# Kernel tuning notes

Measured on AMD Instinct MI355X. Metric: run time of the kernel, lower is better.

Reference implementation:

```python
import jax, jax.numpy as jnp
import numpy as np

N = 100_000   # nodes
E = 1_600_000 # edges (avg degree 16)
D = 64        # embed/hidden dim
V = 50_000    # vocab
G = 128       # graphs in batch
C = 20        # classes


def setup_inputs() -> dict:
    key = jax.random.key(0)
    ks = jax.random.split(key, 11)
    tokens = jax.random.randint(ks[0], (N,), 0, V)
    edge_src = jax.random.randint(ks[1], (E,), 0, N)
    edge_dst = jax.random.randint(ks[2], (E,), 0, N)
    graph_ids = jnp.sort(jax.random.randint(ks[3], (N,), 0, G))
    s = 1.0 / np.sqrt(D)
    return {
        "tokens": tokens,
        "edge_src": edge_src,
        "edge_dst": edge_dst,
        "graph_ids": graph_ids,
        "emb_table": jax.random.normal(ks[4], (V, D), jnp.float32) * 0.02,
        "W1": jax.random.normal(ks[5], (D, D), jnp.float32) * s,
        "b1": jax.random.normal(ks[6], (D,), jnp.float32) * s,
        "W2": jax.random.normal(ks[7], (D, D), jnp.float32) * s,
        "b2": jax.random.normal(ks[8], (D,), jnp.float32) * s,
        "Wc": jax.random.normal(ks[9], (D, C), jnp.float32) * s,
        "bc": jax.random.normal(ks[10], (C,), jnp.float32) * s,
    }


def reference(tokens, edge_src, edge_dst, graph_ids, emb_table, W1, b1, W2, b2, Wc, bc):
    # Embedding lookup: [N, D]
    h = emb_table[tokens]
    # in-degree per dst node (zero-degree nodes get 0 features, like DGL mean)
    deg = jax.ops.segment_sum(jnp.ones((E,), h.dtype), edge_dst, num_segments=N)
    inv_deg = (1.0 / jnp.maximum(deg, 1.0))[:, None]  # [N,1]

    def gcn(h, W, b):
        # copy_src + mean: gather src feats, segment-sum into dst, divide by degree
        agg = jax.ops.segment_sum(h[edge_src], edge_dst, num_segments=N) * inv_deg
        return jax.nn.relu(agg @ W + b)

    h = gcn(h, W1, b1)
    h = gcn(h, W2, b2)

    # dgl.mean_nodes: per-graph mean pooling
    cnt = jax.ops.segment_sum(jnp.ones((N,), h.dtype), graph_ids, num_segments=G)
    hg = jax.ops.segment_sum(h, graph_ids, num_segments=G) / jnp.maximum(cnt, 1.0)[:, None]
    return hg @ Wc + bc  # [G, C] logits
```

## Files before the change

### kernel.cpp

```cpp
#include <hip/hip_runtime.h>

#define DIM 64
#define CLS 20
#define SCAN_T 256
#define SCAN_E 1024

__global__ void deg_count_kernel(const int* __restrict__ edst, int* __restrict__ deg, int E) {
    int e = blockIdx.x * blockDim.x + threadIdx.x;
    if (e < E) atomicAdd(&deg[edst[e]], 1);
}

__global__ void scan1_kernel(const int* __restrict__ deg, int* __restrict__ rp,
                             int* __restrict__ bsum, int N) {
    __shared__ int sh[SCAN_T];
    int base = blockIdx.x * SCAN_E + threadIdx.x * 4;
    int v0 = (base + 0 < N) ? deg[base + 0] : 0;
    int v1 = (base + 1 < N) ? deg[base + 1] : 0;
    int v2 = (base + 2 < N) ? deg[base + 2] : 0;
    int v3 = (base + 3 < N) ? deg[base + 3] : 0;
    sh[threadIdx.x] = v0 + v1 + v2 + v3;
    __syncthreads();
    for (int off = 1; off < SCAN_T; off <<= 1) {
        int t = (threadIdx.x >= off) ? sh[threadIdx.x - off] : 0;
        __syncthreads();
        sh[threadIdx.x] += t;
        __syncthreads();
    }
    int run = (threadIdx.x > 0) ? sh[threadIdx.x - 1] : 0;
    if (base + 0 < N) rp[base + 0] = run; run += v0;
    if (base + 1 < N) rp[base + 1] = run; run += v1;
    if (base + 2 < N) rp[base + 2] = run; run += v2;
    if (base + 3 < N) rp[base + 3] = run;
    if (threadIdx.x == SCAN_T - 1) bsum[blockIdx.x] = sh[SCAN_T - 1];
}

__global__ void scan2_kernel(int* __restrict__ bsum, int NB) {
    __shared__ int sh[128];
    int v = (threadIdx.x < NB) ? bsum[threadIdx.x] : 0;
    sh[threadIdx.x] = v;
    __syncthreads();
    for (int off = 1; off < 128; off <<= 1) {
        int t = (threadIdx.x >= off) ? sh[threadIdx.x - off] : 0;
        __syncthreads();
        sh[threadIdx.x] += t;
        __syncthreads();
    }
    if (threadIdx.x < NB) bsum[threadIdx.x] = sh[threadIdx.x] - v;
}

__global__ void scan3_kernel(int* __restrict__ rp, const int* __restrict__ bsum, int N) {
    int i = blockIdx.x * blockDim.x + threadIdx.x;
    if (i < N) rp[i] += bsum[i >> 10];
}

__global__ void scatter_kernel(const int* __restrict__ esrc, const int* __restrict__ edst,
                               int* __restrict__ cursor, int* __restrict__ csr_src, int E) {
    int e = blockIdx.x * blockDim.x + threadIdx.x;
    if (e < E) {
        int pos = atomicAdd(&cursor[edst[e]], 1);
        csr_src[pos] = esrc[e];
    }
}

__global__ void embed_kernel(const int* __restrict__ tokens, const float* __restrict__ emb,
                             float* __restrict__ h, int N) {
    int t = blockIdx.x * blockDim.x + threadIdx.x;
    int n = t >> 4, c = t & 15;
    if (n < N) {
        int tok = tokens[n];
        ((float4*)h)[(size_t)n * 16 + c] = ((const float4*)emb)[(size_t)tok * 16 + c];
    }
}

__global__ void agg_csr_kernel(const int* __restrict__ rp, const int* __restrict__ deg,
                               const int* __restrict__ csr_src, const float* __restrict__ h,
                               float* __restrict__ agg, int N) {
    int t = blockIdx.x * blockDim.x + threadIdx.x;
    int n = t >> 4, c = t & 15;
    if (n >= N) return;
    int beg = rp[n], end = beg + deg[n];
    float ax = 0.f, ay = 0.f, az = 0.f, aw = 0.f;
    for (int e = beg; e < end; ++e) {
        int s = csr_src[e];
        float4 v = ((const float4*)h)[(size_t)s * 16 + c];
        ax += v.x; ay += v.y; az += v.z; aw += v.w;
    }
    float4 o = {ax, ay, az, aw};
    ((float4*)agg)[(size_t)n * 16 + c] = o;
}

__global__ void gemm_relu_kernel(const float* __restrict__ agg, const int* __restrict__ deg,
                                 const float* __restrict__ W, const float* __restrict__ b,
                                 float* __restrict__ out, int N) {
    __shared__ float4 Ws[64 * 16];
    __shared__ float4 bs[16];
    for (int i = threadIdx.x; i < 64 * 16; i += blockDim.x) Ws[i] = ((const float4*)W)[i];
    if (threadIdx.x < 16) bs[threadIdx.x] = ((const float4*)b)[threadIdx.x];
    __syncthreads();
    int n = blockIdx.x * blockDim.x + threadIdx.x;
    if (n >= N) return;
    float inv = 1.0f / fmaxf((float)deg[n], 1.0f);
    float4 hv[16];
    #pragma unroll
    for (int j = 0; j < 16; ++j) hv[j] = ((const float4*)agg)[(size_t)n * 16 + j];
    float4 acc[16];
    #pragma unroll
    for (int j = 0; j < 16; ++j) { acc[j].x = 0.f; acc[j].y = 0.f; acc[j].z = 0.f; acc[j].w = 0.f; }
    #pragma unroll
    for (int k4 = 0; k4 < 16; ++k4) {
        float4 hq = hv[k4];
        #pragma unroll
        for (int kk = 0; kk < 4; ++kk) {
            float hk = (kk == 0) ? hq.x : (kk == 1) ? hq.y : (kk == 2) ? hq.z : hq.w;
            int k = k4 * 4 + kk;
            #pragma unroll
            for (int j = 0; j < 16; ++j) {
                float4 w = Ws[k * 16 + j];
                acc[j].x = fmaf(hk, w.x, acc[j].x);
                acc[j].y = fmaf(hk, w.y, acc[j].y);
                acc[j].z = fmaf(hk, w.z, acc[j].z);
                acc[j].w = fmaf(hk, w.w, acc[j].w);
            }
        }
    }
    #pragma unroll
    for (int j = 0; j < 16; ++j) {
        float4 bb = bs[j];
        float4 o;
        o.x = fmaxf(fmaf(inv, acc[j].x, bb.x), 0.f);
        o.y = fmaxf(fmaf(inv, acc[j].y, bb.y), 0.f);
        o.z = fmaxf(fmaf(inv, acc[j].z, bb.z), 0.f);
        o.w = fmaxf(fmaf(inv, acc[j].w, bb.w), 0.f);
        ((float4*)out)[(size_t)n * 16 + j] = o;
    }
}

__device__ __forceinline__ int lower_bound_i(const int* a, int n, int key) {
    int lo = 0, hi = n;
    while (lo < hi) {
        int mid = (lo + hi) >> 1;
        if (a[mid] < key) lo = mid + 1; else hi = mid;
    }
    return lo;
}

__global__ void pool_head_kernel(const float* __restrict__ h, const int* __restrict__ gids,
                                 const float* __restrict__ Wc, const float* __restrict__ bc,
                                 float* __restrict__ out, int N) {
    __shared__ float4 red[256];
    __shared__ float hg[64];
    int g = blockIdx.x;
    int lo = lower_bound_i(gids, N, g);
    int hi = lower_bound_i(gids, N, g + 1);
    int r = threadIdx.x >> 4, c = threadIdx.x & 15;
    float ax = 0.f, ay = 0.f, az = 0.f, aw = 0.f;
    for (int n = lo + r; n < hi; n += 16) {
        float4 v = ((const float4*)h)[(size_t)n * 16 + c];
        ax += v.x; ay += v.y; az += v.z; aw += v.w;
    }
    float4 a = {ax, ay, az, aw};
    red[threadIdx.x] = a;
    __syncthreads();
    for (int s = 8; s > 0; s >>= 1) {
        if (r < s) {
            float4 m = red[r * 16 + c];
            float4 o = red[(r + s) * 16 + c];
            m.x += o.x; m.y += o.y; m.z += o.z; m.w += o.w;
            red[r * 16 + c] = m;
        }
        __syncthreads();
    }
    if (r == 0) {
        float icnt = 1.0f / fmaxf((float)(hi - lo), 1.0f);
        float4 m = red[c];
        hg[c * 4 + 0] = m.x * icnt;
        hg[c * 4 + 1] = m.y * icnt;
        hg[c * 4 + 2] = m.z * icnt;
        hg[c * 4 + 3] = m.w * icnt;
    }
    __syncthreads();
    if (threadIdx.x < CLS) {
        float s = bc[threadIdx.x];
        #pragma unroll
        for (int k = 0; k < 64; ++k) s = fmaf(hg[k], Wc[k * CLS + threadIdx.x], s);
        out[(size_t)g * CLS + threadIdx.x] = s;
    }
}

extern "C" void kernel_launch(void* const* d_in, const int* in_sizes, int n_in,
                              void* d_out, int out_size, void* d_ws, size_t ws_size,
                              hipStream_t stream) {
    const int*   tokens = (const int*)d_in[0];
    const int*   esrc   = (const int*)d_in[1];
    const int*   edst   = (const int*)d_in[2];
    const int*   gids   = (const int*)d_in[3];
    const float* emb    = (const float*)d_in[4];
    const float* W1     = (const float*)d_in[5];
    const float* b1     = (const float*)d_in[6];
    const float* W2     = (const float*)d_in[7];
    const float* b2     = (const float*)d_in[8];
    const float* Wc     = (const float*)d_in[9];
    const float* bc     = (const float*)d_in[10];
    int N = in_sizes[0];
    int E = in_sizes[1];
    float* out = (float*)d_out;

    float* h      = (float*)d_ws;
    float* agg    = h + (size_t)N * 64;
    int*   deg    = (int*)(agg + (size_t)N * 64);
    int*   rp     = deg + N;
    int*   cursor = rp + N;
    int*   csr    = cursor + N;
    int*   bsum   = csr + E;

    int NB = (N + SCAN_E - 1) / SCAN_E;

    hipMemsetAsync(deg, 0, (size_t)N * sizeof(int), stream);

    deg_count_kernel<<<(E + 255) / 256, 256, 0, stream>>>(edst, deg, E);
    scan1_kernel<<<NB, SCAN_T, 0, stream>>>(deg, rp, bsum, N);
    scan2_kernel<<<1, 128, 0, stream>>>(bsum, NB);
    scan3_kernel<<<(N + 255) / 256, 256, 0, stream>>>(rp, bsum, N);
    hipMemcpyAsync(cursor, rp, (size_t)N * sizeof(int), hipMemcpyDeviceToDevice, stream);
    scatter_kernel<<<(E + 255) / 256, 256, 0, stream>>>(esrc, edst, cursor, csr, E);

    embed_kernel<<<(N * 16 + 255) / 256, 256, 0, stream>>>(tokens, emb, h, N);

    agg_csr_kernel<<<(N * 16 + 255) / 256, 256, 0, stream>>>(rp, deg, csr, h, agg, N);
    gemm_relu_kernel<<<(N + 255) / 256, 256, 0, stream>>>(agg, deg, W1, b1, h, N);

    agg_csr_kernel<<<(N * 16 + 255) / 256, 256, 0, stream>>>(rp, deg, csr, h, agg, N);
    gemm_relu_kernel<<<(N + 255) / 256, 256, 0, stream>>>(agg, deg, W2, b2, h, N);

    pool_head_kernel<<<128, 256, 0, stream>>>(h, gids, Wc, bc, out, N);
}
```

Baseline: 512.8 us.

## Partition degree count and CSR scatter atomics into destination bands

```diff
diff --git a/kernel.cpp b/kernel.cpp
--- a/kernel.cpp
+++ b/kernel.cpp
@@ -4,10 +4,46 @@
 #define CLS 20
 #define SCAN_T 256
 #define SCAN_E 1024
-
-__global__ void deg_count_kernel(const int* __restrict__ edst, int* __restrict__ deg, int E) {
-    int e = blockIdx.x * blockDim.x + threadIdx.x;
-    if (e < E) atomicAdd(&deg[edst[e]], 1);
+#define NBANDS 8
+#define BBLOCKS 1024
+
+__global__ void banded_count_kernel(const int* __restrict__ edst, int* __restrict__ deg,
+                                    int N, int E) {
+    int band   = blockIdx.x & (NBANDS - 1);
+    int chunk  = blockIdx.x >> 3;
+    int nchunk = gridDim.x >> 3;
+    int bandSize = (N + NBANDS - 1) / NBANDS;
+    int lo = band * bandSize;
+    int hi = min(lo + bandSize, N);
+    int per  = (E + nchunk - 1) / nchunk;
+    int ebeg = chunk * per;
+    int eend = min(ebeg + per, E);
+    for (int e = ebeg + threadIdx.x; e < eend; e += blockDim.x) {
+        int d = edst[e];
+        if (d >= lo && d < hi) atomicAdd(&deg[d], 1);
+    }
+}
+
+__global__ void banded_scatter_kernel(const int* __restrict__ esrc, const int* __restrict__ edst,
+                                      int* __restrict__ cursor, int* __restrict__ csr_src,
+                                      int N, int E) {
+    int band   = blockIdx.x & (NBANDS - 1);
+    int chunk  = blockIdx.x >> 3;
+    int nchunk = gridDim.x >> 3;
+    int bandSize = (N + NBANDS - 1) / NBANDS;
+    int lo = band * bandSize;
+    int hi = min(lo + bandSize, N);
+    int per  = (E + nchunk - 1) / nchunk;
+    int ebeg = chunk * per;
+    int eend = min(ebeg + per, E);
+    for (int e = ebeg + threadIdx.x; e < eend; e += blockDim.x) {
+        int d = edst[e];
+        int s = esrc[e];
+        if (d >= lo && d < hi) {
+            int pos = atomicAdd(&cursor[d], 1);
+            csr_src[pos] = s;
+        }
+    }
 }
 
 __global__ void scan1_kernel(const int* __restrict__ deg, int* __restrict__ rp,
@@ -48,17 +84,13 @@
     if (threadIdx.x < NB) bsum[threadIdx.x] = sh[threadIdx.x] - v;
 }
 
-__global__ void scan3_kernel(int* __restrict__ rp, const int* __restrict__ bsum, int N) {
+__global__ void scan3_kernel(int* __restrict__ rp, int* __restrict__ cursor,
+                             const int* __restrict__ bsum, int N) {
     int i = blockIdx.x * blockDim.x + threadIdx.x;
-    if (i < N) rp[i] += bsum[i >> 10];
-}
-
-__global__ void scatter_kernel(const int* __restrict__ esrc, const int* __restrict__ edst,
-                               int* __restrict__ cursor, int* __restrict__ csr_src, int E) {
-    int e = blockIdx.x * blockDim.x + threadIdx.x;
-    if (e < E) {
-        int pos = atomicAdd(&cursor[edst[e]], 1);
-        csr_src[pos] = esrc[e];
+    if (i < N) {
+        int v = rp[i] + bsum[i >> 10];
+        rp[i] = v;
+        cursor[i] = v;
     }
 }
 
@@ -217,12 +249,11 @@
 
     hipMemsetAsync(deg, 0, (size_t)N * sizeof(int), stream);
 
-    deg_count_kernel<<<(E + 255) / 256, 256, 0, stream>>>(edst, deg, E);
+    banded_count_kernel<<<BBLOCKS, 256, 0, stream>>>(edst, deg, N, E);
     scan1_kernel<<<NB, SCAN_T, 0, stream>>>(deg, rp, bsum, N);
     scan2_kernel<<<1, 128, 0, stream>>>(bsum, NB);
-    scan3_kernel<<<(N + 255) / 256, 256, 0, stream>>>(rp, bsum, N);
-    hipMemcpyAsync(cursor, rp, (size_t)N * sizeof(int), hipMemcpyDeviceToDevice, stream);
-    scatter_kernel<<<(E + 255) / 256, 256, 0, stream>>>(esrc, edst, cursor, csr, E);
+    scan3_kernel<<<(N + 255) / 256, 256, 0, stream>>>(rp, cursor, bsum, N);
+    banded_scatter_kernel<<<BBLOCKS, 256, 0, stream>>>(esrc, edst, cursor, csr, N, E);
 
     embed_kernel<<<(N * 16 + 255) / 256, 256, 0, stream>>>(tokens, emb, h, N);
 
```

Measured after the change: 459.8 us. -10.3%, faster.

## Replace CSR build with bucketed edge queues and fuse aggregation with GEMM

Applied to the files above, without the earlier changes.

```diff
diff --git a/kernel.cpp b/kernel.cpp
--- a/kernel.cpp
+++ b/kernel.cpp
@@ -2,63 +2,37 @@
 
 #define DIM 64
 #define CLS 20
-#define SCAN_T 256
-#define SCAN_E 1024
-
-__global__ void deg_count_kernel(const int* __restrict__ edst, int* __restrict__ deg, int E) {
-    int e = blockIdx.x * blockDim.x + threadIdx.x;
-    if (e < E) atomicAdd(&deg[edst[e]], 1);
-}
-
-__global__ void scan1_kernel(const int* __restrict__ deg, int* __restrict__ rp,
-                             int* __restrict__ bsum, int N) {
-    __shared__ int sh[SCAN_T];
-    int base = blockIdx.x * SCAN_E + threadIdx.x * 4;
-    int v0 = (base + 0 < N) ? deg[base + 0] : 0;
-    int v1 = (base + 1 < N) ? deg[base + 1] : 0;
-    int v2 = (base + 2 < N) ? deg[base + 2] : 0;
-    int v3 = (base + 3 < N) ? deg[base + 3] : 0;
-    sh[threadIdx.x] = v0 + v1 + v2 + v3;
-    __syncthreads();
-    for (int off = 1; off < SCAN_T; off <<= 1) {
-        int t = (threadIdx.x >= off) ? sh[threadIdx.x - off] : 0;
-        __syncthreads();
-        sh[threadIdx.x] += t;
-        __syncthreads();
-    }
-    int run = (threadIdx.x > 0) ? sh[threadIdx.x - 1] : 0;
-    if (base + 0 < N) rp[base + 0] = run; run += v0;
-    if (base + 1 < N) rp[base + 1] = run; run += v1;
-    if (base + 2 < N) rp[base + 2] = run; run += v2;
-    if (base + 3 < N) rp[base + 3] = run;
-    if (threadIdx.x == SCAN_T - 1) bsum[blockIdx.x] = sh[SCAN_T - 1];
-}
-
-__global__ void scan2_kernel(int* __restrict__ bsum, int NB) {
-    __shared__ int sh[128];
-    int v = (threadIdx.x < NB) ? bsum[threadIdx.x] : 0;
-    sh[threadIdx.x] = v;
-    __syncthreads();
-    for (int off = 1; off < 128; off <<= 1) {
-        int t = (threadIdx.x >= off) ? sh[threadIdx.x - off] : 0;
-        __syncthreads();
-        sh[threadIdx.x] += t;
-        __syncthreads();
-    }
-    if (threadIdx.x < NB) bsum[threadIdx.x] = sh[threadIdx.x] - v;
-}
-
-__global__ void scan3_kernel(int* __restrict__ rp, const int* __restrict__ bsum, int N) {
-    int i = blockIdx.x * blockDim.x + threadIdx.x;
-    if (i < N) rp[i] += bsum[i >> 10];
-}
-
-__global__ void scatter_kernel(const int* __restrict__ esrc, const int* __restrict__ edst,
-                               int* __restrict__ cursor, int* __restrict__ csr_src, int E) {
-    int e = blockIdx.x * blockDim.x + threadIdx.x;
-    if (e < E) {
-        int pos = atomicAdd(&cursor[edst[e]], 1);
-        csr_src[pos] = esrc[e];
+#define BSZ 160
+#define MAXBND 640
+#define QCAP 3072
+#define PCHUNK 4096
+#define ASTRIDE 68
+
+__global__ void init_qcur_kernel(int* __restrict__ qcur, int nbnd) {
+    int i = threadIdx.x;
+    if (i < nbnd) qcur[i] = i * QCAP;
+}
+
+__global__ __launch_bounds__(512) void partition_kernel(
+        const int* __restrict__ esrc, const int* __restrict__ edst,
+        int2* __restrict__ queue, int* __restrict__ qcur, int nbnd, int E) {
+    __shared__ int hist[MAXBND];
+    __shared__ int pc[MAXBND];
+    int cbeg = blockIdx.x * PCHUNK;
+    int cend = min(cbeg + PCHUNK, E);
+    for (int i = threadIdx.x; i < nbnd; i += blockDim.x) hist[i] = 0;
+    __syncthreads();
+    for (int e = cbeg + threadIdx.x; e < cend; e += blockDim.x)
+        atomicAdd(&hist[edst[e] / BSZ], 1);
+    __syncthreads();
+    for (int i = threadIdx.x; i < nbnd; i += blockDim.x)
+        pc[i] = hist[i] ? atomicAdd(&qcur[i], hist[i]) : 0;
+    __syncthreads();
+    for (int e = cbeg + threadIdx.x; e < cend; e += blockDim.x) {
+        int d = edst[e];
+        int s = esrc[e];
+        int pos = atomicAdd(&pc[d / BSZ], 1);
+        queue[pos] = make_int2(s, d);
     }
 }
 
@@ -72,66 +46,87 @@
     }
 }
 
-__global__ void agg_csr_kernel(const int* __restrict__ rp, const int* __restrict__ deg,
-                               const int* __restrict__ csr_src, const float* __restrict__ h,
-                               float* __restrict__ agg, int N) {
-    int t = blockIdx.x * blockDim.x + threadIdx.x;
-    int n = t >> 4, c = t & 15;
-    if (n >= N) return;
-    int beg = rp[n], end = beg + deg[n];
-    float ax = 0.f, ay = 0.f, az = 0.f, aw = 0.f;
-    for (int e = beg; e < end; ++e) {
-        int s = csr_src[e];
-        float4 v = ((const float4*)h)[(size_t)s * 16 + c];
-        ax += v.x; ay += v.y; az += v.z; aw += v.w;
-    }
-    float4 o = {ax, ay, az, aw};
-    ((float4*)agg)[(size_t)n * 16 + c] = o;
-}
-
-__global__ void gemm_relu_kernel(const float* __restrict__ agg, const int* __restrict__ deg,
-                                 const float* __restrict__ W, const float* __restrict__ b,
-                                 float* __restrict__ out, int N) {
+__global__ __launch_bounds__(512) void fused_layer_kernel(
+        const int2* __restrict__ queue, const int* __restrict__ qcur,
+        const float* __restrict__ hin, const float* __restrict__ W,
+        const float* __restrict__ bias, float* __restrict__ hout, int N) {
+    __shared__ float  acc[BSZ * ASTRIDE];
+    __shared__ int    ldeg[BSZ];
     __shared__ float4 Ws[64 * 16];
-    __shared__ float4 bs[16];
-    for (int i = threadIdx.x; i < 64 * 16; i += blockDim.x) Ws[i] = ((const float4*)W)[i];
-    if (threadIdx.x < 16) bs[threadIdx.x] = ((const float4*)b)[threadIdx.x];
-    __syncthreads();
-    int n = blockIdx.x * blockDim.x + threadIdx.x;
-    if (n >= N) return;
-    float inv = 1.0f / fmaxf((float)deg[n], 1.0f);
-    float4 hv[16];
-    #pragma unroll
-    for (int j = 0; j < 16; ++j) hv[j] = ((const float4*)agg)[(size_t)n * 16 + j];
-    float4 acc[16];
-    #pragma unroll
-    for (int j = 0; j < 16; ++j) { acc[j].x = 0.f; acc[j].y = 0.f; acc[j].z = 0.f; acc[j].w = 0.f; }
-    #pragma unroll
-    for (int k4 = 0; k4 < 16; ++k4) {
-        float4 hq = hv[k4];
-        #pragma unroll
-        for (int kk = 0; kk < 4; ++kk) {
-            float hk = (kk == 0) ? hq.x : (kk == 1) ? hq.y : (kk == 2) ? hq.z : hq.w;
-            int k = k4 * 4 + kk;
+    __shared__ float4 bs4[16];
+    int tid = threadIdx.x;
+
+    for (int i = tid; i < BSZ * (ASTRIDE / 4); i += blockDim.x) {
+        float4 z = {0.f, 0.f, 0.f, 0.f};
+        int r = i / (ASTRIDE / 4), q = i % (ASTRIDE / 4);
+        *(float4*)&acc[r * ASTRIDE + q * 4] = z;
+    }
+    for (int i = tid; i < BSZ; i += blockDim.x) ldeg[i] = 0;
+    for (int i = tid; i < 64 * 16; i += blockDim.x) Ws[i] = ((const float4*)W)[i];
+    if (tid < 16) bs4[tid] = ((const float4*)bias)[tid];
+    __syncthreads();
+
+    int b = blockIdx.x;
+    int nbase = b * BSZ;
+    int qbeg = b * QCAP;
+    int qend = qcur[b];
+    int slot = tid >> 4, c = tid & 15;
+
+    int e = qbeg + slot;
+    for (; e + 32 < qend; e += 64) {
+        int2 e0 = queue[e];
+        int2 e1 = queue[e + 32];
+        float4 v0 = ((const float4*)hin)[(size_t)e0.x * 16 + c];
+        float4 v1 = ((const float4*)hin)[(size_t)e1.x * 16 + c];
+        float* a0 = &acc[(e0.y - nbase) * ASTRIDE + c * 4];
+        atomicAdd(a0 + 0, v0.x); atomicAdd(a0 + 1, v0.y);
+        atomicAdd(a0 + 2, v0.z); atomicAdd(a0 + 3, v0.w);
+        if (c == 0) atomicAdd(&ldeg[e0.y - nbase], 1);
+        float* a1 = &acc[(e1.y - nbase) * ASTRIDE + c * 4];
+        atomicAdd(a1 + 0, v1.x); atomicAdd(a1 + 1, v1.y);
+        atomicAdd(a1 + 2, v1.z); atomicAdd(a1 + 3, v1.w);
+        if (c == 0) atomicAdd(&ldeg[e1.y - nbase], 1);
+    }
+    if (e < qend) {
+        int2 e0 = queue[e];
+        float4 v0 = ((const float4*)hin)[(size_t)e0.x * 16 + c];
+        float* a0 = &acc[(e0.y - nbase) * ASTRIDE + c * 4];
+        atomicAdd(a0 + 0, v0.x); atomicAdd(a0 + 1, v0.y);
+        atomicAdd(a0 + 2, v0.z); atomicAdd(a0 + 3, v0.w);
+        if (c == 0) atomicAdd(&ldeg[e0.y - nbase], 1);
+    }
+    __syncthreads();
+
+    for (int r0 = 0; r0 < BSZ; r0 += 32) {
+        int r = r0 + slot;
+        int n = nbase + r;
+        if (n < N) {
+            float inv = 1.0f / fmaxf((float)ldeg[r], 1.0f);
+            float sx = 0.f, sy = 0.f, sz = 0.f, sw = 0.f;
             #pragma unroll
-            for (int j = 0; j < 16; ++j) {
-                float4 w = Ws[k * 16 + j];
-                acc[j].x = fmaf(hk, w.x, acc[j].x);
-                acc[j].y = fmaf(hk, w.y, acc[j].y);
-                acc[j].z = fmaf(hk, w.z, acc[j].z);
-                acc[j].w = fmaf(hk, w.w, acc[j].w);
+            for (int k4 = 0; k4 < 16; ++k4) {
+                float4 aq = *(const float4*)&acc[r * ASTRIDE + k4 * 4];
+                float4 w0 = Ws[(k4 * 4 + 0) * 16 + c];
+                float4 w1 = Ws[(k4 * 4 + 1) * 16 + c];
+                float4 w2 = Ws[(k4 * 4 + 2) * 16 + c];
+                float4 w3 = Ws[(k4 * 4 + 3) * 16 + c];
+                sx = fmaf(aq.x, w0.x, sx); sy = fmaf(aq.x, w0.y, sy);
+                sz = fmaf(aq.x, w0.z, sz); sw = fmaf(aq.x, w0.w, sw);
+                sx = fmaf(aq.y, w1.x, sx); sy = fmaf(aq.y, w1.y, sy);
+                sz = fmaf(aq.y, w1.z, sz); sw = fmaf(aq.y, w1.w, sw);
+                sx = fmaf(aq.z, w2.x, sx); sy = fmaf(aq.z, w2.y, sy);
+                sz = fmaf(aq.z, w2.z, sz); sw = fmaf(aq.z, w2.w, sw);
+                sx = fmaf(aq.w, w3.x, sx); sy = fmaf(aq.w, w3.y, sy);
+                sz = fmaf(aq.w, w3.z, sz); sw = fmaf(aq.w, w3.w, sw);
             }
+            float4 bb = bs4[c];
+            float4 o;
+            o.x = fmaxf(fmaf(inv, sx, bb.x), 0.f);
+            o.y = fmaxf(fmaf(inv, sy, bb.y), 0.f);
+            o.z = fmaxf(fmaf(inv, sz, bb.z), 0.f);
+            o.w = fmaxf(fmaf(inv, sw, bb.w), 0.f);
+            ((float4*)hout)[(size_t)n * 16 + c] = o;
         }
-    }
-    #pragma unroll
-    for (int j = 0; j < 16; ++j) {
-        float4 bb = bs[j];
-        float4 o;
-        o.x = fmaxf(fmaf(inv, acc[j].x, bb.x), 0.f);
-        o.y = fmaxf(fmaf(inv, acc[j].y, bb.y), 0.f);
-        o.z = fmaxf(fmaf(inv, acc[j].z, bb.z), 0.f);
-        o.w = fmaxf(fmaf(inv, acc[j].w, bb.w), 0.f);
-        ((float4*)out)[(size_t)n * 16 + j] = o;
     }
 }
 
@@ -205,32 +200,17 @@
     int E = in_sizes[1];
     float* out = (float*)d_out;
 
-    float* h      = (float*)d_ws;
-    float* agg    = h + (size_t)N * 64;
-    int*   deg    = (int*)(agg + (size_t)N * 64);
-    int*   rp     = deg + N;
-    int*   cursor = rp + N;
-    int*   csr    = cursor + N;
-    int*   bsum   = csr + E;
-
-    int NB = (N + SCAN_E - 1) / SCAN_E;
-
-    hipMemsetAsync(deg, 0, (size_t)N * sizeof(int), stream);
-
-    deg_count_kernel<<<(E + 255) / 256, 256, 0, stream>>>(edst, deg, E);
-    scan1_kernel<<<NB, SCAN_T, 0, stream>>>(deg, rp, bsum, N);
-    scan2_kernel<<<1, 128, 0, stream>>>(bsum, NB);
-    scan3_kernel<<<(N + 255) / 256, 256, 0, stream>>>(rp, bsum, N);
-    hipMemcpyAsync(cursor, rp, (size_t)N * sizeof(int), hipMemcpyDeviceToDevice, stream);
-    scatter_kernel<<<(E + 255) / 256, 256, 0, stream>>>(esrc, edst, cursor, csr, E);
-
-    embed_kernel<<<(N * 16 + 255) / 256, 256, 0, stream>>>(tokens, emb, h, N);
-
-    agg_csr_kernel<<<(N * 16 + 255) / 256, 256, 0, stream>>>(rp, deg, csr, h, agg, N);
-    gemm_relu_kernel<<<(N + 255) / 256, 256, 0, stream>>>(agg, deg, W1, b1, h, N);
-
-    agg_csr_kernel<<<(N * 16 + 255) / 256, 256, 0, stream>>>(rp, deg, csr, h, agg, N);
-    gemm_relu_kernel<<<(N + 255) / 256, 256, 0, stream>>>(agg, deg, W2, b2, h, N);
-
-    pool_head_kernel<<<128, 256, 0, stream>>>(h, gids, Wc, bc, out, N);
-}
+    int nbnd = (N + BSZ - 1) / BSZ;
+
+    float* hA    = (float*)d_ws;
+    float* hB    = hA + (size_t)N * 64;
+    int2*  queue = (int2*)(hB + (size_t)N * 64);
+    int*   qcur  = (int*)(queue + (size_t)MAXBND * QCAP);
+
+    init_qcur_kernel<<<1, MAXBND, 0, stream>>>(qcur, nbnd);
+    partition_kernel<<<(E + PCHUNK - 1) / PCHUNK, 512, 0, stream>>>(esrc, edst, queue, qcur, nbnd, E);
+    embed_kernel<<<(N * 16 + 255) / 256, 256, 0, stream>>>(tokens, emb, hA, N);
+    fused_layer_kernel<<<nbnd, 512, 0, stream>>>(queue, qcur, hA, W1, b1, hB, N);
+    fused_layer_kernel<<<nbnd, 512, 0, stream>>>(queue, qcur, hB, W2, b2, hA, N);
+    pool_head_kernel<<<128, 256, 0, stream>>>(hA, gids, Wc, bc, out, N);
+}
```

Result: slower. 1.464 ms (+185.5%).
